# Optimization experiments

Measured on AMD Instinct MI355X. Metric: run time of the kernel, lower is better.

The kernel has to match this reference:

```python
import jax, jax.numpy as jnp
import numpy as np

B, SD, SE = 4, 2048, 2048
HID, HID_ = 300, 512
N_HEADS = 8


def setup_inputs() -> dict:
    key = jax.random.key(0)
    ks = jax.random.split(key, 7)
    en = jax.random.normal(ks[0], (B, SE, HID), dtype=jnp.float32)
    de = jax.random.normal(ks[1], (B, SD, HID), dtype=jnp.float32)
    mask = jax.random.randint(ks[2], (1, 1, SD, SE), 0, 2).astype(jnp.bool_)
    WQ = jax.random.normal(ks[3], (HID, HID_), dtype=jnp.float32)
    WK = jax.random.normal(ks[4], (HID, HID_), dtype=jnp.float32)
    WV = jax.random.normal(ks[5], (HID, HID_), dtype=jnp.float32)
    WO = jax.random.normal(ks[6], (HID_, HID), dtype=jnp.float32)
    return {"en": en, "de": de, "mask": mask, "WQ": WQ, "WK": WK, "WV": WV, "WO": WO}


def reference(en, de, mask, WQ, WK, WV, WO):
    # Faithful to the torch module (dropout in eval mode => identity).
    d_k = de.shape[-1]  # NOTE: original scales by sqrt(hidden_dim)=sqrt(300), not head_dim
    b_d, s_d = de.shape[0], de.shape[1]
    b_e, s_e = en.shape[0], en.shape[1]
    # head axis is the LAST axis of the reshape (size 8), exactly as the original view/permute
    q = jnp.transpose((de @ WQ).reshape(b_d, s_d, -1, N_HEADS), (3, 0, 1, 2))  # [8,B,Sd,64]
    k = jnp.transpose((en @ WK).reshape(b_e, s_e, -1, N_HEADS), (3, 0, 2, 1))  # [8,B,64,Se]
    v = jnp.transpose((en @ WV).reshape(b_e, s_e, -1, N_HEADS), (3, 0, 1, 2))  # [8,B,Se,64]
    e = jnp.matmul(q, k) / jnp.sqrt(jnp.asarray(d_k, dtype=q.dtype))           # [8,B,Sd,Se]
    e = jnp.where(mask, jnp.asarray(-1e9, dtype=e.dtype), e)
    alpha = jax.nn.softmax(e, axis=3)
    head3 = jnp.matmul(alpha, v)                                               # [8,B,Sd,64]
    # torch.cat((head3[0],...,head3[7]), 2) == move head axis into feature concat order
    a = jnp.concatenate([head3[h] for h in range(N_HEADS)], axis=2)            # [B,Sd,512]
    return a @ WO                                                              # [B,Sd,300]
```

## Files before the change

### kernel.cpp

```cpp
#include <hip/hip_runtime.h>
#include <hip/hip_bf16.h>
#include <math.h>

#define B_      4
#define SD_     2048
#define SE_     2048
#define HIDIN   300
#define HIDMID  512
#define NH      8
#define DH      64
#define ESZ     ((size_t)4194304)
#define BUFB    24576

typedef __attribute__((ext_vector_type(8))) short          s16x8;
typedef __attribute__((ext_vector_type(8))) unsigned short u16x8;
typedef __attribute__((ext_vector_type(4))) unsigned short u16x4;
typedef __attribute__((ext_vector_type(4))) float          f32x4;

#define MFMA16 __builtin_amdgcn_mfma_f32_16x16x32_bf16

#define QSCALE  0.0832940411f
#define NEGL   -1.4426950e9f

__device__ __forceinline__ unsigned short f2bf(float f) {
    unsigned int u = __float_as_uint(f);
    u += 0x7fffu + ((u >> 16) & 1u);
    return (unsigned short)(u >> 16);
}
__device__ __forceinline__ float bf2f(unsigned short s) {
    return __uint_as_float((unsigned int)s << 16);
}
__device__ __forceinline__ void gload16(const void* g, void* l) {
    __builtin_amdgcn_global_load_lds(
        (const __attribute__((address_space(1))) void*)g,
        (__attribute__((address_space(3))) void*)l, 16, 0, 0);
}

#define OF_QH   ((size_t)0)
#define OF_QL   (ESZ)
#define OF_KH   (2*ESZ)
#define OF_KL   (3*ESZ)
#define OF_VT   (4*ESZ)
#define OF_BB   (5*ESZ)
#define OF_CA   (5*ESZ + 262144)
#define OF_CW   (OF_CA + 10485760)
#define OF_WOT  (OF_CW + 983040)

__global__ __launch_bounds__(256) void bias_kernel(const int* __restrict__ mask,
                                                   unsigned long long* __restrict__ BiasB)
{
    const int idx = blockIdx.x * 256 + threadIdx.x;
    const int q = idx >> 5, tile = idx & 31;
    const int* __restrict__ mrow = mask + (size_t)q * SE_ + tile * 64;
    unsigned long long w = 0;
#pragma unroll
    for (int sub = 0; sub < 4; ++sub)
#pragma unroll
        for (int gv = 0; gv < 4; ++gv) {
            const int4 mm = *(const int4*)(mrow + sub * 16 + gv * 4);
            const int bp = gv * 16 + sub * 4;
            if (mm.x) w |= 1ull << bp;
            if (mm.y) w |= 1ull << (bp + 1);
            if (mm.z) w |= 1ull << (bp + 2);
            if (mm.w) w |= 1ull << (bp + 3);
        }
    BiasB[idx] = w;
}

__global__ __launch_bounds__(256) void convA_kernel(
    const float* __restrict__ de, const float* __restrict__ en,
    unsigned short* __restrict__ CA)
{
    const int idx = blockIdx.x * 256 + threadIdx.x;
    const int mat = blockIdx.y;
    const float* __restrict__ A = mat ? en : de;
    unsigned short* __restrict__ H = CA + (size_t)mat * 5242880;
    unsigned short* __restrict__ L = H + 2621440;
    const int row = idx / 10, ch = idx - row * 10;
    float v[32];
    if (ch < 9) {
#pragma unroll
        for (int i = 0; i < 8; ++i) {
            const float4 f = *(const float4*)(A + (size_t)row * 300 + ch * 32 + i * 4);
            v[i*4+0] = f.x; v[i*4+1] = f.y; v[i*4+2] = f.z; v[i*4+3] = f.w;
        }
    } else {
#pragma unroll
        for (int i = 0; i < 32; ++i) {
            const int k = 288 + i;
            v[i] = (k < 300) ? A[(size_t)row * 300 + k] : 0.f;
        }
    }
    const int r128 = row & 127;
    const int xr = (r128 >> 1) & 3;
    const size_t tb = ((size_t)(row >> 7) * 10 + ch) * 4096 + r128 * 32;
#pragma unroll
    for (int sub = 0; sub < 4; ++sub) {
        const int slot = sub ^ xr;
        u16x8 hv, lv;
#pragma unroll
        for (int e = 0; e < 8; ++e) {
            const float f = v[sub * 8 + e];
            const unsigned short h = f2bf(f);
            hv[e] = h; lv[e] = f2bf(f - bf2f(h));
        }
        *(u16x8*)(H + tb + slot * 8) = hv;
        *(u16x8*)(L + tb + slot * 8) = lv;
    }
}

__global__ __launch_bounds__(256) void convW_kernel(
    const float* __restrict__ WQ, const float* __restrict__ WK,
    const float* __restrict__ WV, const float* __restrict__ WO,
    unsigned short* __restrict__ CW, unsigned short* __restrict__ WOT)
{
    const int idx = blockIdx.x * 256 + threadIdx.x;
    if (idx < 122880) {
        const int which = idx / 40960;
        const int rem = idx - which * 40960;
        const int k = rem >> 7;
        const int n0 = (rem & 127) * 4;
        const float* __restrict__ W = which == 0 ? WQ : (which == 1 ? WK : WV);
        unsigned short* __restrict__ H = CW + (size_t)which * 327680;
        unsigned short* __restrict__ L = H + 163840;
        const float sc = (which == 0) ? QSCALE : 1.f;
        float4 w = make_float4(0.f, 0.f, 0.f, 0.f);
        if (k < 300) w = *(const float4*)(W + (size_t)k * 512 + n0);
        const float wv4[4] = {w.x * sc, w.y * sc, w.z * sc, w.w * sc};
        const int ch = k >> 5, kk = k & 31;
#pragma unroll
        for (int j = 0; j < 4; ++j) {
            const int n = n0 + j, ntile = n >> 7, nr = n & 127;
            const size_t o = ((size_t)(ntile * 10 + ch) * 128 + nr) * 32
                           + (((kk >> 3) ^ ((nr >> 1) & 3)) << 3) + (kk & 7);
            const unsigned short h = f2bf(wv4[j]);
            H[o] = h; L[o] = f2bf(wv4[j] - bf2f(h));
        }
    } else {
        const int idx2 = idx - 122880;
        const int k = idx2 / 96, n4 = idx2 - k * 96;
        const int n0 = n4 * 4;
        float4 w = make_float4(0.f, 0.f, 0.f, 0.f);
        if (n0 < 300) w = *(const float4*)(WO + (size_t)k * 300 + n0);
        const float wv4[4] = {w.x, w.y, w.z, w.w};
        const int ch = k >> 5, kk = k & 31;
#pragma unroll
        for (int j = 0; j < 4; ++j) {
            const int n = n0 + j, ntile = n >> 7, nr = n & 127;
            const size_t o = ((size_t)(ntile * 16 + ch) * 128 + nr) * 32
                           + (((kk >> 3) ^ ((nr >> 1) & 3)) << 3) + (kk & 7);
            WOT[o] = f2bf(wv4[j]);
        }
    }
}

__global__ __launch_bounds__(256) void proj_mfma_kernel(
    const unsigned short* __restrict__ CA, const unsigned short* __restrict__ CW,
    unsigned short* __restrict__ Qh, unsigned short* __restrict__ Ql,
    unsigned short* __restrict__ KhT, unsigned short* __restrict__ KlT,
    unsigned short* __restrict__ VtT)
{
    const int stile = blockIdx.x, jtile = blockIdx.y, which = blockIdx.z;
    const int tid = threadIdx.x, wv = tid >> 6, lane = tid & 63;
    const int li = lane & 15, g = lane >> 4;
    const int wr = wv >> 1, wc = wv & 1;

    __shared__ __align__(16) char LBp[65536];

    const unsigned short* __restrict__ pAh =
        CA + (size_t)(which ? 1 : 0) * 5242880 + (size_t)stile * 40960 + tid * 8;
    const unsigned short* __restrict__ pAl = pAh + 2621440;
    const unsigned short* __restrict__ pWh =
        CW + (size_t)which * 327680 + (size_t)jtile * 40960 + tid * 8;
    const unsigned short* __restrict__ pWl = pWh + 163840;

#define STAGEP(ch, bofs) {                                                    \
        char* db = LBp + (bofs) + wv * 1024;                                  \
        const size_t co = (size_t)(ch) * 4096;                                \
        gload16(pAh + co,        db);                                         \
        gload16(pAh + co + 2048, db + 4096);                                  \
        gload16(pAl + co,        db + 8192);                                  \
        gload16(pAl + co + 2048, db + 12288);                                 \
        gload16(pWh + co,        db + 16384);                                 \
        gload16(pWh + co + 2048, db + 20480);                                 \
        gload16(pWl + co,        db + 24576);                                 \
        gload16(pWl + co + 2048, db + 28672);                                 \
    }

    int offA[4], offW[4];
#pragma unroll
    for (int ssub = 0; ssub < 4; ++ssub) {
        const int r = wr * 64 + ssub * 16 + li;
        offA[ssub] = r * 64 + ((g ^ ((r >> 1) & 3)) << 4);
    }
#pragma unroll
    for (int jsub = 0; jsub < 4; ++jsub) {
        const int n = wc * 64 + jsub * 16 + li;
        offW[jsub] = n * 64 + ((g ^ ((n >> 1) & 3)) << 4);
    }

    f32x4 acc[4][4];
#pragma unroll
    for (int i = 0; i < 4; ++i)
#pragma unroll
        for (int j = 0; j < 4; ++j) acc[i][j] = (f32x4){0.f, 0.f, 0.f, 0.f};

    STAGEP(0, 0)
    __syncthreads();

#pragma unroll 1
    for (int ch = 0; ch < 10; ++ch) {
        const int bofs = (ch & 1) * 32768;
        if (ch < 9) STAGEP(ch + 1, bofs ^ 32768)
        const char* bp = LBp + bofs;
        s16x8 ah[4], al[4], wh[4], wl[4];
#pragma unroll
        for (int ssub = 0; ssub < 4; ++ssub) {
            ah[ssub] = *(const s16x8*)(bp + offA[ssub]);
            al[ssub] = *(const s16x8*)(bp + 8192 + offA[ssub]);
        }
#pragma unroll
        for (int jsub = 0; jsub < 4; ++jsub) {
            wh[jsub] = *(const s16x8*)(bp + 16384 + offW[jsub]);
            wl[jsub] = *(const s16x8*)(bp + 24576 + offW[jsub]);
        }
#pragma unroll
        for (int ssub = 0; ssub < 4; ++ssub)
#pragma unroll
            for (int jsub = 0; jsub < 4; ++jsub) {
                acc[ssub][jsub] = MFMA16(ah[ssub], wh[jsub], acc[ssub][jsub], 0, 0, 0);
                acc[ssub][jsub] = MFMA16(ah[ssub], wl[jsub], acc[ssub][jsub], 0, 0, 0);
                acc[ssub][jsub] = MFMA16(al[ssub], wh[jsub], acc[ssub][jsub], 0, 0, 0);
            }
        __syncthreads();
    }
#undef STAGEP

    const int jgbase = jtile * 128 + wc * 64 + li;
    const int sbase0 = stile * 128 + wr * 64 + 4 * g;
#pragma unroll
    for (int jsub = 0; jsub < 4; ++jsub) {
        const int jgg = jgbase + jsub * 16;
        const int d = jgg >> 3, hh = jgg & 7;
#pragma unroll
        for (int ssub = 0; ssub < 4; ++ssub) {
            const f32x4 v = acc[ssub][jsub];
            const int sg0 = sbase0 + ssub * 16;
            const int bbv = sg0 >> 11;
            const int bhn = bbv * 8 + hh;
            const int sl0 = sg0 & 2047;
            if (which == 0) {
                const size_t o = ((size_t)bhn * 2048 + sl0) * 64 + d;
#pragma unroll
                for (int r = 0; r < 4; ++r) {
                    const float val = v[r];
                    const unsigned short hi = f2bf(val);
                    Qh[o + r * 64] = hi;
                    Ql[o + r * 64] = f2bf(val - bf2f(hi));
                }
            } else if (which == 1) {
                const int tile = sl0 >> 6, tt0 = sl0 & 63;
                const size_t tb = ((size_t)(bhn * 32 + tile)) << 12;
#pragma unroll
                for (int r = 0; r < 4; ++r) {
                    const int tt = tt0 + r;
                    const size_t o = tb + tt * 64 + (((d >> 3) ^ (tt & 7)) << 3) + (d & 7);
                    const float val = v[r];
                    const unsigned short hi = f2bf(val);
                    KhT[o] = hi;
                    KlT[o] = f2bf(val - bf2f(hi));
                }
            } else {
                const int tile = sl0 >> 6, tin0 = sl0 & 63;
                const size_t tb = ((size_t)(bhn * 32 + tile)) << 12;
                const int blk = tin0 >> 5, gg2 = (tin0 >> 2) & 3, half = (tin0 >> 4) & 1;
                const size_t o = tb + (size_t)d * 64
                               + ((((blk << 2) | gg2) ^ (d & 7)) << 3) + half * 4;
                u16x4 pk;
#pragma unroll
                for (int r = 0; r < 4; ++r) pk[r] = f2bf(v[r]);
                *(u16x4*)(VtT + o) = pk;
            }
        }
    }
}

__global__ __launch_bounds__(512, 4) void attn_mfma_kernel(
    const unsigned short* __restrict__ Qh, const unsigned short* __restrict__ Ql,
    const unsigned short* __restrict__ KhT, const unsigned short* __restrict__ KlT,
    const unsigned short* __restrict__ VtT, const unsigned short* __restrict__ BiasP,
    unsigned short* __restrict__ AOb)
{
    const int qt = blockIdx.x, bh = blockIdx.y;
    const int bb = bh >> 3, hh = bh & 7;
    const int tid = threadIdx.x;
    const int wv = tid >> 6, lane = tid & 63;
    const int g = lane >> 4, li = lane & 15;
    const int q = qt * 128 + wv * 16 + li;

    __shared__ __align__(16) char LB[2 * BUFB];

    const size_t qoff = ((size_t)bh * SD_ + q) * DH + 8 * g;
    const s16x8 qh0 = *(const s16x8*)(Qh + qoff);
    const s16x8 qh1 = *(const s16x8*)(Qh + qoff + 32);
    const s16x8 ql0 = *(const s16x8*)(Ql + qoff);
    const s16x8 ql1 = *(const s16x8*)(Ql + qoff + 32);

    const unsigned short* __restrict__ sKh = KhT + ((size_t)bh << 17) + tid * 8;
    const unsigned short* __restrict__ sKl = KlT + ((size_t)bh << 17) + tid * 8;
    const unsigned short* __restrict__ sVt = VtT + ((size_t)bh << 17) + tid * 8;

    const int base0 = li * 128 + ((g ^ (li & 7)) << 4);
    const int base1 = li * 128 + (((4 + g) ^ (li & 7)) << 4);

#define STAGE(tile, boff)                                                     \
    {                                                                         \
        char* db = LB + (boff) + wv * 1024;                                   \
        const size_t toff = (size_t)(tile) << 12;                             \
        gload16(sKh + toff, db);                                              \
        gload16(sKl + toff, db + 8192);                                       \
        gload16(sVt + toff, db + 16384);                                      \
    }

    float m = -INFINITY, l = 0.f;
    f32x4 O[4];
#pragma unroll
    for (int i = 0; i < 4; ++i) O[i] = (f32x4){0.f, 0.f, 0.f, 0.f};

    STAGE(0, 0)
    unsigned short bw = BiasP[(size_t)q * 128 + g];
    __syncthreads();

    int bufoff = 0;
#pragma unroll 1
    for (int it = 0; it < 32; ++it) {
        const int nxt = (it + 1) & 31;
        STAGE(nxt, bufoff ^ BUFB)
        const unsigned short bwN = BiasP[(size_t)q * 128 + nxt * 4 + g];

        f32x4 s[4];
#pragma unroll
        for (int sub = 0; sub < 4; ++sub)
#pragma unroll
            for (int c = 0; c < 4; ++c)
                s[sub][c] = ((bw >> (sub * 4 + c)) & 1) ? NEGL : 0.f;

#pragma unroll
        for (int sub = 0; sub < 4; ++sub) {
            const s16x8 kh0 = *(const s16x8*)(LB + bufoff + base0 + sub * 2048);
            const s16x8 kh1 = *(const s16x8*)(LB + bufoff + base1 + sub * 2048);
            const s16x8 kl0 = *(const s16x8*)(LB + bufoff + base0 + 8192 + sub * 2048);
            const s16x8 kl1 = *(const s16x8*)(LB + bufoff + base1 + 8192 + sub * 2048);
            s[sub] = MFMA16(kh0, qh0, s[sub], 0, 0, 0);
            s[sub] = MFMA16(kh0, ql0, s[sub], 0, 0, 0);
            s[sub] = MFMA16(kl0, qh0, s[sub], 0, 0, 0);
            s[sub] = MFMA16(kh1, qh1, s[sub], 0, 0, 0);
            s[sub] = MFMA16(kh1, ql1, s[sub], 0, 0, 0);
            s[sub] = MFMA16(kl1, qh1, s[sub], 0, 0, 0);
        }

        float tmax = fmaxf(fmaxf(s[0][0], s[0][1]), fmaxf(s[0][2], s[0][3]));
        tmax = fmaxf(tmax, fmaxf(fmaxf(s[1][0], s[1][1]), fmaxf(s[1][2], s[1][3])));
        tmax = fmaxf(tmax, fmaxf(fmaxf(s[2][0], s[2][1]), fmaxf(s[2][2], s[2][3])));
        tmax = fmaxf(tmax, fmaxf(fmaxf(s[3][0], s[3][1]), fmaxf(s[3][2], s[3][3])));
        tmax = fmaxf(tmax, __shfl_xor(tmax, 16));
        tmax = fmaxf(tmax, __shfl_xor(tmax, 32));
        const float mn  = fmaxf(m, tmax);
        const float scl = exp2f(m - mn);
        float ps = 0.f;
#pragma unroll
        for (int sub = 0; sub < 4; ++sub)
#pragma unroll
            for (int c = 0; c < 4; ++c) {
                float p = exp2f(s[sub][c] - mn);
                s[sub][c] = p;
                ps += p;
            }
        ps += __shfl_xor(ps, 16);
        ps += __shfl_xor(ps, 32);
        l = l * scl + ps;
        m = mn;
#pragma unroll
        for (int i = 0; i < 4; ++i) O[i] *= scl;

        union { s16x8 v; unsigned int w[4]; } P0, P1;
        asm("v_cvt_pk_bf16_f32 %0, %1, %2" : "=v"(P0.w[0]) : "v"(s[0][0]), "v"(s[0][1]));
        asm("v_cvt_pk_bf16_f32 %0, %1, %2" : "=v"(P0.w[1]) : "v"(s[0][2]), "v"(s[0][3]));
        asm("v_cvt_pk_bf16_f32 %0, %1, %2" : "=v"(P0.w[2]) : "v"(s[1][0]), "v"(s[1][1]));
        asm("v_cvt_pk_bf16_f32 %0, %1, %2" : "=v"(P0.w[3]) : "v"(s[1][2]), "v"(s[1][3]));
        asm("v_cvt_pk_bf16_f32 %0, %1, %2" : "=v"(P1.w[0]) : "v"(s[2][0]), "v"(s[2][1]));
        asm("v_cvt_pk_bf16_f32 %0, %1, %2" : "=v"(P1.w[1]) : "v"(s[2][2]), "v"(s[2][3]));
        asm("v_cvt_pk_bf16_f32 %0, %1, %2" : "=v"(P1.w[2]) : "v"(s[3][0]), "v"(s[3][1]));
        asm("v_cvt_pk_bf16_f32 %0, %1, %2" : "=v"(P1.w[3]) : "v"(s[3][2]), "v"(s[3][3]));

#pragma unroll
        for (int dsub = 0; dsub < 4; ++dsub) {
            const s16x8 vf0 = *(const s16x8*)(LB + bufoff + base0 + 16384 + dsub * 2048);
            const s16x8 vf1 = *(const s16x8*)(LB + bufoff + base1 + 16384 + dsub * 2048);
            O[dsub] = MFMA16(vf0, P0.v, O[dsub], 0, 0, 0);
            O[dsub] = MFMA16(vf1, P1.v, O[dsub], 0, 0, 0);
        }

        bw = bwN;
        __syncthreads();
        bufoff ^= BUFB;
    }

    const float rl = 1.f / l;
    const int row = bb * 2048 + q;
    const int r128 = row & 127;
    const int xr = (r128 >> 1) & 3;
    unsigned short* __restrict__ ab = AOb + ((size_t)(row >> 7)) * 65536
                                    + r128 * 32 + (g & 1) * 4;
#pragma unroll
    for (int dsub = 0; dsub < 4; ++dsub) {
        const f32x4 o = O[dsub] * rl;
        const int ch = hh * 2 + (dsub >> 1);
        const int slot = ((dsub & 1) * 2 + (g >> 1)) ^ xr;
        u16x4 pk;
#pragma unroll
        for (int c = 0; c < 4; ++c) pk[c] = f2bf(o[c]);
        *(u16x4*)(ab + (size_t)ch * 4096 + slot * 8) = pk;
    }
#undef STAGE
}

__global__ __launch_bounds__(256) void epi_mfma_kernel(
    const unsigned short* __restrict__ AOb, const unsigned short* __restrict__ WOT,
    float* __restrict__ out)
{
    const int stile = blockIdx.x, jtile = blockIdx.y;
    const int tid = threadIdx.x, wv = tid >> 6, lane = tid & 63;
    const int li = lane & 15, g = lane >> 4;
    const int wr = wv >> 1, wc = wv & 1;

    __shared__ __align__(16) char LBe[32768];

    const unsigned short* __restrict__ pA = AOb + (size_t)stile * 65536 + tid * 8;
    const unsigned short* __restrict__ pW = WOT + (size_t)jtile * 65536 + tid * 8;

#define STAGEE(ch, bofs) {                                                    \
        char* db = LBe + (bofs) + wv * 1024;                                  \
        const size_t co = (size_t)(ch) * 4096;                                \
        gload16(pA + co,        db);                                          \
        gload16(pA + co + 2048, db + 4096);                                   \
        gload16(pW + co,        db + 8192);                                   \
        gload16(pW + co + 2048, db + 12288);                                  \
    }

    int offA[4], offW[4];
#pragma unroll
    for (int ssub = 0; ssub < 4; ++ssub) {
        const int r = wr * 64 + ssub * 16 + li;
        offA[ssub] = r * 64 + ((g ^ ((r >> 1) & 3)) << 4);
    }
#pragma unroll
    for (int jsub = 0; jsub < 4; ++jsub) {
        const int n = wc * 64 + jsub * 16 + li;
        offW[jsub] = n * 64 + ((g ^ ((n >> 1) & 3)) << 4);
    }

    f32x4 acc[4][4];
#pragma unroll
    for (int i = 0; i < 4; ++i)
#pragma unroll
        for (int j = 0; j < 4; ++j) acc[i][j] = (f32x4){0.f, 0.f, 0.f, 0.f};

    STAGEE(0, 0)
    __syncthreads();

#pragma unroll 1
    for (int ch = 0; ch < 16; ++ch) {
        const int bofs = (ch & 1) * 16384;
        if (ch < 15) STAGEE(ch + 1, bofs ^ 16384)
        const char* bp = LBe + bofs;
        s16x8 ah[4], wh[4];
#pragma unroll
        for (int ssub = 0; ssub < 4; ++ssub)
            ah[ssub] = *(const s16x8*)(bp + offA[ssub]);
#pragma unroll
        for (int jsub = 0; jsub < 4; ++jsub)
            wh[jsub] = *(const s16x8*)(bp + 8192 + offW[jsub]);
#pragma unroll
        for (int ssub = 0; ssub < 4; ++ssub)
#pragma unroll
            for (int jsub = 0; jsub < 4; ++jsub)
                acc[ssub][jsub] = MFMA16(ah[ssub], wh[jsub], acc[ssub][jsub], 0, 0, 0);
        __syncthreads();
    }
#undef STAGEE

    const int jgbase = jtile * 128 + wc * 64 + li;
    const int sbase0 = stile * 128 + wr * 64 + 4 * g;
#pragma unroll
    for (int jsub = 0; jsub < 4; ++jsub) {
        const int o = jgbase + jsub * 16;
        if (o < HIDIN) {
#pragma unroll
            for (int ssub = 0; ssub < 4; ++ssub) {
                const f32x4 v = acc[ssub][jsub];
                const int sg0 = sbase0 + ssub * 16;
#pragma unroll
                for (int r = 0; r < 4; ++r)
                    out[(size_t)(sg0 + r) * HIDIN + o] = v[r];
            }
        }
    }
}

extern "C" void kernel_launch(void* const* d_in, const int* in_sizes, int n_in,
                              void* d_out, int out_size, void* d_ws, size_t ws_size,
                              hipStream_t stream)
{
    const float* en  = (const float*)d_in[0];
    const float* de  = (const float*)d_in[1];
    const int*   mask = (const int*)d_in[2];
    const float* WQ  = (const float*)d_in[3];
    const float* WK  = (const float*)d_in[4];
    const float* WV  = (const float*)d_in[5];
    const float* WO  = (const float*)d_in[6];
    float* out = (float*)d_out;

    unsigned short* ws2 = (unsigned short*)d_ws;
    unsigned short* Qh  = ws2 + OF_QH;
    unsigned short* Ql  = ws2 + OF_QL;
    unsigned short* KhT = ws2 + OF_KH;
    unsigned short* KlT = ws2 + OF_KL;
    unsigned short* VtT = ws2 + OF_VT;
    unsigned long long* BiasB = (unsigned long long*)(ws2 + OF_BB);
    unsigned short* CA  = ws2 + OF_CA;
    unsigned short* CW  = ws2 + OF_CW;
    unsigned short* WOT = ws2 + OF_WOT;
    unsigned short* AOb = CA;

    bias_kernel<<<dim3(256), 256, 0, stream>>>(mask, BiasB);
    convA_kernel<<<dim3(320, 2), 256, 0, stream>>>(de, en, CA);
    convW_kernel<<<dim3(672), 256, 0, stream>>>(WQ, WK, WV, WO, CW, WOT);
    proj_mfma_kernel<<<dim3(64, 4, 3), 256, 0, stream>>>(CA, CW, Qh, Ql, KhT, KlT, VtT);
    attn_mfma_kernel<<<dim3(16, 32), 512, 0, stream>>>(Qh, Ql, KhT, KlT, VtT,
                                                       (const unsigned short*)BiasB, AOb);
    epi_mfma_kernel<<<dim3(64, 3), 256, 0, stream>>>(AOb, WOT, out);
}
```

Measured before the change: 192.1 us.

## Triple-buffer attention K/V, defer softmax rescale, retile epilogue, add MFMA priority

```diff
diff --git a/kernel.cpp b/kernel.cpp
--- a/kernel.cpp
+++ b/kernel.cpp
@@ -21,6 +21,7 @@
 
 #define QSCALE  0.0832940411f
 #define NEGL   -1.4426950e9f
+#define DEFER_THR 24.0f
 
 __device__ __forceinline__ unsigned short f2bf(float f) {
     unsigned int u = __float_as_uint(f);
@@ -224,6 +225,7 @@
             wh[jsub] = *(const s16x8*)(bp + 16384 + offW[jsub]);
             wl[jsub] = *(const s16x8*)(bp + 24576 + offW[jsub]);
         }
+        __builtin_amdgcn_s_setprio(1);
 #pragma unroll
         for (int ssub = 0; ssub < 4; ++ssub)
 #pragma unroll
@@ -232,6 +234,7 @@
                 acc[ssub][jsub] = MFMA16(ah[ssub], wl[jsub], acc[ssub][jsub], 0, 0, 0);
                 acc[ssub][jsub] = MFMA16(al[ssub], wh[jsub], acc[ssub][jsub], 0, 0, 0);
             }
+        __builtin_amdgcn_s_setprio(0);
         __syncthreads();
     }
 #undef STAGEP
@@ -291,14 +294,16 @@
     const unsigned short* __restrict__ VtT, const unsigned short* __restrict__ BiasP,
     unsigned short* __restrict__ AOb)
 {
-    const int qt = blockIdx.x, bh = blockIdx.y;
+    const int lin = blockIdx.x + 16 * blockIdx.y;
+    const int qt = (lin >> 3) & 15;
+    const int bh = (lin & 7) + ((lin >> 7) << 3);
     const int bb = bh >> 3, hh = bh & 7;
     const int tid = threadIdx.x;
     const int wv = tid >> 6, lane = tid & 63;
     const int g = lane >> 4, li = lane & 15;
     const int q = qt * 128 + wv * 16 + li;
 
-    __shared__ __align__(16) char LB[2 * BUFB];
+    __shared__ __align__(16) char LB[3 * BUFB];
 
     const size_t qoff = ((size_t)bh * SD_ + q) * DH + 8 * g;
     const s16x8 qh0 = *(const s16x8*)(Qh + qoff);
@@ -328,15 +333,17 @@
     for (int i = 0; i < 4; ++i) O[i] = (f32x4){0.f, 0.f, 0.f, 0.f};
 
     STAGE(0, 0)
+    STAGE(1, BUFB)
     unsigned short bw = BiasP[(size_t)q * 128 + g];
-    __syncthreads();
-
-    int bufoff = 0;
+    asm volatile("s_waitcnt vmcnt(3)" ::: "memory");
+    __builtin_amdgcn_s_barrier();
+    __builtin_amdgcn_sched_barrier(0);
+
+    int cc = 0, cs = 2 * BUFB;
 #pragma unroll 1
     for (int it = 0; it < 32; ++it) {
-        const int nxt = (it + 1) & 31;
-        STAGE(nxt, bufoff ^ BUFB)
-        const unsigned short bwN = BiasP[(size_t)q * 128 + nxt * 4 + g];
+        STAGE((it + 2) & 31, cs)
+        const unsigned short bwN = BiasP[(size_t)q * 128 + (((it + 1) & 31) << 2) + g];
 
         f32x4 s[4];
 #pragma unroll
@@ -345,12 +352,13 @@
             for (int c = 0; c < 4; ++c)
                 s[sub][c] = ((bw >> (sub * 4 + c)) & 1) ? NEGL : 0.f;
 
+        __builtin_amdgcn_s_setprio(1);
 #pragma unroll
         for (int sub = 0; sub < 4; ++sub) {
-            const s16x8 kh0 = *(const s16x8*)(LB + bufoff + base0 + sub * 2048);
-            const s16x8 kh1 = *(const s16x8*)(LB + bufoff + base1 + sub * 2048);
-            const s16x8 kl0 = *(const s16x8*)(LB + bufoff + base0 + 8192 + sub * 2048);
-            const s16x8 kl1 = *(const s16x8*)(LB + bufoff + base1 + 8192 + sub * 2048);
+            const s16x8 kh0 = *(const s16x8*)(LB + cc + base0 + sub * 2048);
+            const s16x8 kh1 = *(const s16x8*)(LB + cc + base1 + sub * 2048);
+            const s16x8 kl0 = *(const s16x8*)(LB + cc + base0 + 8192 + sub * 2048);
+            const s16x8 kl1 = *(const s16x8*)(LB + cc + base1 + 8192 + sub * 2048);
             s[sub] = MFMA16(kh0, qh0, s[sub], 0, 0, 0);
             s[sub] = MFMA16(kh0, ql0, s[sub], 0, 0, 0);
             s[sub] = MFMA16(kl0, qh0, s[sub], 0, 0, 0);
@@ -358,30 +366,42 @@
             s[sub] = MFMA16(kh1, ql1, s[sub], 0, 0, 0);
             s[sub] = MFMA16(kl1, qh1, s[sub], 0, 0, 0);
         }
+        __builtin_amdgcn_s_setprio(0);
 
         float tmax = fmaxf(fmaxf(s[0][0], s[0][1]), fmaxf(s[0][2], s[0][3]));
         tmax = fmaxf(tmax, fmaxf(fmaxf(s[1][0], s[1][1]), fmaxf(s[1][2], s[1][3])));
         tmax = fmaxf(tmax, fmaxf(fmaxf(s[2][0], s[2][1]), fmaxf(s[2][2], s[2][3])));
         tmax = fmaxf(tmax, fmaxf(fmaxf(s[3][0], s[3][1]), fmaxf(s[3][2], s[3][3])));
-        tmax = fmaxf(tmax, __shfl_xor(tmax, 16));
-        tmax = fmaxf(tmax, __shfl_xor(tmax, 32));
-        const float mn  = fmaxf(m, tmax);
-        const float scl = exp2f(m - mn);
-        float ps = 0.f;
-#pragma unroll
-        for (int sub = 0; sub < 4; ++sub)
-#pragma unroll
-            for (int c = 0; c < 4; ++c) {
-                float p = exp2f(s[sub][c] - mn);
-                s[sub][c] = p;
-                ps += p;
-            }
-        ps += __shfl_xor(ps, 16);
-        ps += __shfl_xor(ps, 32);
-        l = l * scl + ps;
-        m = mn;
-#pragma unroll
-        for (int i = 0; i < 4; ++i) O[i] *= scl;
+        if (__all(tmax <= m + DEFER_THR)) {
+            float ps = 0.f;
+#pragma unroll
+            for (int sub = 0; sub < 4; ++sub)
+#pragma unroll
+                for (int c = 0; c < 4; ++c) {
+                    float p = exp2f(s[sub][c] - m);
+                    s[sub][c] = p;
+                    ps += p;
+                }
+            l += ps;
+        } else {
+            tmax = fmaxf(tmax, __shfl_xor(tmax, 16));
+            tmax = fmaxf(tmax, __shfl_xor(tmax, 32));
+            const float mn  = fmaxf(m, tmax);
+            const float scl = exp2f(m - mn);
+            float ps = 0.f;
+#pragma unroll
+            for (int sub = 0; sub < 4; ++sub)
+#pragma unroll
+                for (int c = 0; c < 4; ++c) {
+                    float p = exp2f(s[sub][c] - mn);
+                    s[sub][c] = p;
+                    ps += p;
+                }
+            l = l * scl + ps;
+            m = mn;
+#pragma unroll
+            for (int i = 0; i < 4; ++i) O[i] *= scl;
+        }
 
         union { s16x8 v; unsigned int w[4]; } P0, P1;
         asm("v_cvt_pk_bf16_f32 %0, %1, %2" : "=v"(P0.w[0]) : "v"(s[0][0]), "v"(s[0][1]));
@@ -393,19 +413,26 @@
         asm("v_cvt_pk_bf16_f32 %0, %1, %2" : "=v"(P1.w[2]) : "v"(s[3][0]), "v"(s[3][1]));
         asm("v_cvt_pk_bf16_f32 %0, %1, %2" : "=v"(P1.w[3]) : "v"(s[3][2]), "v"(s[3][3]));
 
+        __builtin_amdgcn_s_setprio(1);
 #pragma unroll
         for (int dsub = 0; dsub < 4; ++dsub) {
-            const s16x8 vf0 = *(const s16x8*)(LB + bufoff + base0 + 16384 + dsub * 2048);
-            const s16x8 vf1 = *(const s16x8*)(LB + bufoff + base1 + 16384 + dsub * 2048);
+            const s16x8 vf0 = *(const s16x8*)(LB + cc + base0 + 16384 + dsub * 2048);
+            const s16x8 vf1 = *(const s16x8*)(LB + cc + base1 + 16384 + dsub * 2048);
             O[dsub] = MFMA16(vf0, P0.v, O[dsub], 0, 0, 0);
             O[dsub] = MFMA16(vf1, P1.v, O[dsub], 0, 0, 0);
         }
+        __builtin_amdgcn_s_setprio(0);
 
         bw = bwN;
-        __syncthreads();
-        bufoff ^= BUFB;
-    }
-
+        asm volatile("s_waitcnt vmcnt(3)" ::: "memory");
+        __builtin_amdgcn_s_barrier();
+        __builtin_amdgcn_sched_barrier(0);
+        cc += BUFB; if (cc == 3 * BUFB) cc = 0;
+        cs += BUFB; if (cs == 3 * BUFB) cs = 0;
+    }
+
+    l += __shfl_xor(l, 16);
+    l += __shfl_xor(l, 32);
     const float rl = 1.f / l;
     const int row = bb * 2048 + q;
     const int r128 = row & 127;
@@ -432,77 +459,78 @@
     const int stile = blockIdx.x, jtile = blockIdx.y;
     const int tid = threadIdx.x, wv = tid >> 6, lane = tid & 63;
     const int li = lane & 15, g = lane >> 4;
-    const int wr = wv >> 1, wc = wv & 1;
-
-    __shared__ __align__(16) char LBe[32768];
-
-    const unsigned short* __restrict__ pA = AOb + (size_t)stile * 65536 + tid * 8;
+
+    __shared__ __align__(16) char LBe[24576];
+
+    const unsigned short* __restrict__ pA =
+        AOb + (size_t)(stile >> 1) * 65536 + (stile & 1) * 2048 + tid * 8;
     const unsigned short* __restrict__ pW = WOT + (size_t)jtile * 65536 + tid * 8;
 
 #define STAGEE(ch, bofs) {                                                    \
-        char* db = LBe + (bofs) + wv * 1024;                                  \
+        char* dbA = LBe + (bofs) + wv * 1024;                                 \
         const size_t co = (size_t)(ch) * 4096;                                \
-        gload16(pA + co,        db);                                          \
-        gload16(pA + co + 2048, db + 4096);                                   \
-        gload16(pW + co,        db + 8192);                                   \
-        gload16(pW + co + 2048, db + 12288);                                  \
-    }
-
-    int offA[4], offW[4];
+        gload16(pA + co,        dbA);                                         \
+        gload16(pW + co,        dbA + 4096);                                  \
+        gload16(pW + co + 2048, dbA + 8192);                                  \
+    }
+
+    int offA[4], offW[2];
 #pragma unroll
     for (int ssub = 0; ssub < 4; ++ssub) {
-        const int r = wr * 64 + ssub * 16 + li;
+        const int r = ssub * 16 + li;
         offA[ssub] = r * 64 + ((g ^ ((r >> 1) & 3)) << 4);
     }
 #pragma unroll
-    for (int jsub = 0; jsub < 4; ++jsub) {
-        const int n = wc * 64 + jsub * 16 + li;
-        offW[jsub] = n * 64 + ((g ^ ((n >> 1) & 3)) << 4);
-    }
-
-    f32x4 acc[4][4];
+    for (int jsub = 0; jsub < 2; ++jsub) {
+        const int n = wv * 32 + jsub * 16 + li;
+        offW[jsub] = 4096 + n * 64 + ((g ^ ((n >> 1) & 3)) << 4);
+    }
+
+    f32x4 acc[4][2];
 #pragma unroll
     for (int i = 0; i < 4; ++i)
 #pragma unroll
-        for (int j = 0; j < 4; ++j) acc[i][j] = (f32x4){0.f, 0.f, 0.f, 0.f};
+        for (int j = 0; j < 2; ++j) acc[i][j] = (f32x4){0.f, 0.f, 0.f, 0.f};
 
     STAGEE(0, 0)
     __syncthreads();
 
 #pragma unroll 1
     for (int ch = 0; ch < 16; ++ch) {
-        const int bofs = (ch & 1) * 16384;
-        if (ch < 15) STAGEE(ch + 1, bofs ^ 16384)
+        const int bofs = (ch & 1) * 12288;
+        if (ch < 15) STAGEE(ch + 1, bofs ^ 12288)
         const char* bp = LBe + bofs;
-        s16x8 ah[4], wh[4];
+        s16x8 ah[4], wh[2];
 #pragma unroll
         for (int ssub = 0; ssub < 4; ++ssub)
             ah[ssub] = *(const s16x8*)(bp + offA[ssub]);
 #pragma unroll
-        for (int jsub = 0; jsub < 4; ++jsub)
-            wh[jsub] = *(const s16x8*)(bp + 8192 + offW[jsub]);
+        for (int jsub = 0; jsub < 2; ++jsub)
+            wh[jsub] = *(const s16x8*)(bp + offW[jsub]);
+        __builtin_amdgcn_s_setprio(1);
 #pragma unroll
         for (int ssub = 0; ssub < 4; ++ssub)
 #pragma unroll
-            for (int jsub = 0; jsub < 4; ++jsub)
+            for (int jsub = 0; jsub < 2; ++jsub)
                 acc[ssub][jsub] = MFMA16(ah[ssub], wh[jsub], acc[ssub][jsub], 0, 0, 0);
+        __builtin_amdgcn_s_setprio(0);
         __syncthreads();
     }
 #undef STAGEE
 
-    const int jgbase = jtile * 128 + wc * 64 + li;
-    const int sbase0 = stile * 128 + wr * 64 + 4 * g;
-#pragma unroll
-    for (int jsub = 0; jsub < 4; ++jsub) {
-        const int o = jgbase + jsub * 16;
+    const int nbase = jtile * 128 + wv * 32 + li;
+    const int rbase = stile * 64 + 4 * g;
+#pragma unroll
+    for (int jsub = 0; jsub < 2; ++jsub) {
+        const int o = nbase + jsub * 16;
         if (o < HIDIN) {
 #pragma unroll
             for (int ssub = 0; ssub < 4; ++ssub) {
                 const f32x4 v = acc[ssub][jsub];
-                const int sg0 = sbase0 + ssub * 16;
+                const int r0 = rbase + ssub * 16;
 #pragma unroll
                 for (int r = 0; r < 4; ++r)
-                    out[(size_t)(sg0 + r) * HIDIN + o] = v[r];
+                    out[(size_t)(r0 + r) * HIDIN + o] = v[r];
             }
         }
     }
@@ -539,5 +567,5 @@
     proj_mfma_kernel<<<dim3(64, 4, 3), 256, 0, stream>>>(CA, CW, Qh, Ql, KhT, KlT, VtT);
     attn_mfma_kernel<<<dim3(16, 32), 512, 0, stream>>>(Qh, Ql, KhT, KlT, VtT,
                                                        (const unsigned short*)BiasB, AOb);
-    epi_mfma_kernel<<<dim3(64, 3), 256, 0, stream>>>(AOb, WOT, out);
-}
+    epi_mfma_kernel<<<dim3(128, 3), 256, 0, stream>>>(AOb, WOT, out);
+}
```

After: 191.1 us. Within noise of the previous version (-0.5%).
